# Kernel optimization log

Hardware: AMD Instinct MI355X
Metric: run time of the kernel (lower is better)

The kernel has to match this reference:

```python
import math
import jax, jax.numpy as jnp
import numpy as np

B, S, D, H = 4, 2048, 512, 8
DH = D // H
NUM_BUCKETS = 32
MAX_DISTANCE = 128


def _relative_position_bucket(rel_pos, num_buckets=NUM_BUCKETS, max_distance=MAX_DISTANCE):
    # bidirectional T5 bucketing (faithful to the torch staticmethod)
    num_buckets = num_buckets // 2
    rel_buckets = (rel_pos > 0).astype(jnp.int32) * num_buckets
    rel_pos = jnp.abs(rel_pos)
    max_exact = num_buckets // 2
    is_small = rel_pos < max_exact
    # clamp log arg to >=1 element to avoid -inf cast (masked out by is_small anyway)
    rp_f = jnp.maximum(rel_pos, 1).astype(jnp.float32)
    large = max_exact + (
        jnp.log(rp_f / max_exact) / math.log(max_distance / max_exact) * (num_buckets - max_exact)
    ).astype(jnp.int32)
    large = jnp.minimum(large, num_buckets - 1)
    return rel_buckets + jnp.where(is_small, rel_pos, large)


def setup_inputs() -> dict:
    rng = jax.random.key(0)
    ks = jax.random.split(rng, 12)
    s = 0.02
    return {
        'key':   jax.random.normal(ks[0], (B, S, D), jnp.float32),
        'value': jax.random.normal(ks[1], (B, S, D), jnp.float32),
        'query': jax.random.normal(ks[2], (B, S, D), jnp.float32),
        'Wq': jax.random.normal(ks[3], (D, D), jnp.float32) * s,
        'bq': jnp.zeros((D,), jnp.float32),
        'Wk': jax.random.normal(ks[4], (D, D), jnp.float32) * s,
        'bk': jnp.zeros((D,), jnp.float32),
        'Wv': jax.random.normal(ks[5], (D, D), jnp.float32) * s,
        'bv': jnp.zeros((D,), jnp.float32),
        'Wo': jax.random.normal(ks[6], (D, D), jnp.float32) * s,
        'bo': jnp.zeros((D,), jnp.float32),
        'rel_bias': jax.random.normal(ks[7], (NUM_BUCKETS, H), jnp.float32) * s,
        'mask': jax.random.bernoulli(ks[8], 0.5, (B, S, S)),
    }


def reference(key, value, query, Wq, bq, Wk, bk, Wv, bv, Wo, bo, rel_bias, mask):
    def shape(x):  # [B,S,D] -> [B,H,S,DH]
        return x.reshape(B, -1, H, DH).transpose(0, 2, 1, 3)

    q = shape(query @ Wq + bq) / math.sqrt(DH)
    k = shape(key @ Wk + bk)
    v = shape(value @ Wv + bv)

    scores = jnp.einsum('bhqd,bhkd->bhqk', q, k)  # [B,H,S,S]

    # T5 relative position bias
    rel_pos = jnp.arange(S)[None, :] - jnp.arange(S)[:, None]  # [S,S] memory - query
    buckets = _relative_position_bucket(rel_pos)
    pos_bias = rel_bias[buckets]                     # [S,S,H]
    scores = scores + pos_bias.transpose(2, 0, 1)[None]  # [1,H,S,S]

    scores = jnp.where(mask[:, None, :, :], jnp.float32(-1e18), scores)
    attn = jax.nn.softmax(scores, axis=-1)  # dropout p=0 -> identity

    ctx = jnp.einsum('bhqk,bhkd->bhqd', attn, v)
    ctx = ctx.transpose(0, 2, 1, 3).reshape(B, -1, D)
    return ctx @ Wo + bo
```

## Files before the change

### kernel.cpp

```cpp
#include <hip/hip_runtime.h>
#include <hip/hip_bf16.h>
#include <math.h>

#define BB 4
#define SS 2048
#define DD 512
#define HH 8
#define DHH 64
#define KPAD 72
#define GPAD 72
#define LOG2E 1.44269504088896340736f

typedef __attribute__((ext_vector_type(8))) short short8;
typedef __attribute__((ext_vector_type(4))) float f32x4;
typedef __attribute__((ext_vector_type(16))) float f32x16;
typedef __attribute__((ext_vector_type(4))) unsigned short ushort4v;
typedef unsigned short ushort;
typedef unsigned char uchar;
typedef unsigned int u32;
typedef unsigned long long u64;

static __device__ __forceinline__ ushort f2b(float x) {
    __hip_bfloat16 h = __float2bfloat16(x);
    return *reinterpret_cast<ushort*>(&h);
}

__global__ __launch_bounds__(256) void pack_mask_kernel(const void* __restrict__ mask,
                                                        u64* __restrict__ mwords) {
    __shared__ int sflag;
    const int tid = threadIdx.x;
    if (tid == 0) sflag = 0;
    __syncthreads();
    u32 probe = ((const u32*)mask)[tid];
    if (__any(probe > 1u) && (tid & 63) == 0) sflag = 1;
    __syncthreads();
    const bool bytemode = sflag != 0;

    int idx = blockIdx.x * 256 + tid;
    int w = idx & 31;
    int row = idx >> 5;
    u64 bits = 0ull;
    if (bytemode) {
        const uint4* p4 = (const uint4*)((const uchar*)mask + (size_t)row * SS + w * 64);
#pragma unroll
        for (int i = 0; i < 4; ++i) {
            uint4 v = p4[i];
            unsigned int a[4] = {v.x, v.y, v.z, v.w};
#pragma unroll
            for (int j = 0; j < 4; ++j)
#pragma unroll
                for (int byte = 0; byte < 4; ++byte)
                    if ((a[j] >> (byte * 8)) & 0xffu) bits |= 1ull << (i * 16 + j * 4 + byte);
        }
    } else {
        const int4* p4 = (const int4*)((const int*)mask + (size_t)row * SS + w * 64);
#pragma unroll
        for (int i = 0; i < 16; ++i) {
            int4 v = p4[i];
            if (v.x) bits |= 1ull << (i * 4 + 0);
            if (v.y) bits |= 1ull << (i * 4 + 1);
            if (v.z) bits |= 1ull << (i * 4 + 2);
            if (v.w) bits |= 1ull << (i * 4 + 3);
        }
    }
    mwords[idx] = bits;
}

__device__ __forceinline__ int t5_bucket(int rel) {
    int rb = (rel > 0) ? 16 : 0;
    int ap = rel < 0 ? -rel : rel;
    if (ap < 8) return rb + ap;
    float t = logf((float)ap * 0.125f) / 2.77258872985839844f * 8.0f;
    int large = 8 + (int)t;
    if (large > 15) large = 15;
    return rb + large;
}

__global__ __launch_bounds__(256) void bias_table_kernel(const float* __restrict__ rel_bias,
                                                         float* __restrict__ tbl) {
    int i = blockIdx.x * 256 + threadIdx.x;
    int h = i >> 12;
    int d = (i & 4095) - 2047;
    tbl[i] = LOG2E * rel_bias[t5_bucket(d) * HH + h];
}

__global__ __launch_bounds__(256) void wtrans_kernel(const float* __restrict__ W0, const float* __restrict__ W1,
                                                     const float* __restrict__ W2, const float* __restrict__ W3,
                                                     ushort* __restrict__ T0, ushort* __restrict__ T1,
                                                     ushort* __restrict__ T2, ushort* __restrict__ T3) {
    __shared__ float tile[64][65];
    const float* W = blockIdx.z == 0 ? W0 : blockIdx.z == 1 ? W1 : blockIdx.z == 2 ? W2 : W3;
    ushort*     T = blockIdx.z == 0 ? T0 : blockIdx.z == 1 ? T1 : blockIdx.z == 2 ? T2 : T3;
    const int n0 = blockIdx.x * 64, k0 = blockIdx.y * 64;
    const int tr = threadIdx.x >> 4, tc = threadIdx.x & 15;
#pragma unroll
    for (int i = 0; i < 4; ++i) {
        int r = i * 16 + tr;
        float4 v = *(const float4*)&W[(size_t)(k0 + r) * 512 + n0 + tc * 4];
        tile[r][tc * 4 + 0] = v.x; tile[r][tc * 4 + 1] = v.y;
        tile[r][tc * 4 + 2] = v.z; tile[r][tc * 4 + 3] = v.w;
    }
    __syncthreads();
#pragma unroll
    for (int i = 0; i < 4; ++i) {
        int rn = i * 16 + tr;
        ushort4v o;
#pragma unroll
        for (int j = 0; j < 4; ++j) o[j] = f2b(tile[tc * 4 + j][rn]);
        *(ushort4v*)&T[(size_t)(n0 + rn) * 512 + k0 + tc * 4] = o;
    }
}

__global__ __launch_bounds__(256) void qkv_gemm(const float* __restrict__ Xq, const float* __restrict__ Xk,
                                                const float* __restrict__ Xv,
                                                const ushort* __restrict__ Wqt, const ushort* __restrict__ Wkt,
                                                const ushort* __restrict__ Wvt,
                                                const float* __restrict__ bqp, const float* __restrict__ bkp,
                                                const float* __restrict__ bvp,
                                                ushort* __restrict__ Yq, ushort* __restrict__ Yk,
                                                ushort* __restrict__ Yv) {
    __shared__ ushort Als[128 * GPAD];
    __shared__ ushort Bls[128 * GPAD];
    const int z = blockIdx.z;
    const float* A    = z == 0 ? Xq : z == 1 ? Xk : Xv;
    const ushort* Bt  = z == 0 ? Wqt : z == 1 ? Wkt : Wvt;
    const float* bias = z == 0 ? bqp : z == 1 ? bkp : bvp;
    const float scale = z == 0 ? 0.125f * LOG2E : 1.0f;

    const int tid = threadIdx.x;
    const int lane = tid & 63;
    const int wid = tid >> 6;
    const int lq = lane & 15, lg = lane >> 4;
    const int wr = wid >> 1, wc = wid & 1;
    const int bm = blockIdx.x * 128;
    const int bn = blockIdx.y * 128;

    f32x4 acc[4][4];
#pragma unroll
    for (int m = 0; m < 4; ++m)
#pragma unroll
        for (int n = 0; n < 4; ++n) acc[m][n] = (f32x4){0.f, 0.f, 0.f, 0.f};

    const int sr = tid >> 3;
    const int sc = (tid & 7) * 8;

    for (int k0 = 0; k0 < 512; k0 += 64) {
        __syncthreads();
#pragma unroll
        for (int i = 0; i < 4; ++i) {
            int r = sr + i * 32;
            float4 u = *(const float4*)(A + (size_t)(bm + r) * 512 + k0 + sc);
            float4 v = *(const float4*)(A + (size_t)(bm + r) * 512 + k0 + sc + 4);
            short8 av;
            av[0] = (short)f2b(u.x); av[1] = (short)f2b(u.y); av[2] = (short)f2b(u.z); av[3] = (short)f2b(u.w);
            av[4] = (short)f2b(v.x); av[5] = (short)f2b(v.y); av[6] = (short)f2b(v.z); av[7] = (short)f2b(v.w);
            *(short8*)&Als[r * GPAD + sc] = av;
            short8 bv = *(const short8*)(Bt + (size_t)(bn + r) * 512 + k0 + sc);
            *(short8*)&Bls[r * GPAD + sc] = bv;
        }
        __syncthreads();
#pragma unroll
        for (int kk = 0; kk < 2; ++kk) {
            short8 af[4], bf[4];
#pragma unroll
            for (int m = 0; m < 4; ++m)
                af[m] = *(short8*)&Als[(wr * 64 + m * 16 + lq) * GPAD + kk * 32 + lg * 8];
#pragma unroll
            for (int n = 0; n < 4; ++n)
                bf[n] = *(short8*)&Bls[(wc * 64 + n * 16 + lq) * GPAD + kk * 32 + lg * 8];
#pragma unroll
            for (int m = 0; m < 4; ++m)
#pragma unroll
                for (int n = 0; n < 4; ++n)
                    acc[m][n] = __builtin_amdgcn_mfma_f32_16x16x32_bf16(af[m], bf[n], acc[m][n], 0, 0, 0);
        }
    }

    float bv[4];
#pragma unroll
    for (int n = 0; n < 4; ++n) bv[n] = bias[bn + wc * 64 + n * 16 + lq];

    if (z == 2) {
        const int blk = bm >> 11;
        const int s0 = (bm & 2047) + wr * 64 + lg * 4;
#pragma unroll
        for (int m = 0; m < 4; ++m)
#pragma unroll
            for (int n = 0; n < 4; ++n) {
                int col = bn + wc * 64 + n * 16 + lq;
                ushort4v o;
#pragma unroll
                for (int r = 0; r < 4; ++r) o[r] = f2b(acc[m][n][r] + bv[n]);
                *(ushort4v*)&Yv[((size_t)(blk * 512 + col)) * SS + s0 + m * 16] = o;
            }
    } else {
        ushort* Y = z ? Yk : Yq;
#pragma unroll
        for (int m = 0; m < 4; ++m)
#pragma unroll
            for (int r = 0; r < 4; ++r) {
                int row = bm + wr * 64 + m * 16 + lg * 4 + r;
#pragma unroll
                for (int n = 0; n < 4; ++n) {
                    int col = bn + wc * 64 + n * 16 + lq;
                    Y[(size_t)row * 512 + col] = f2b((acc[m][n][r] + bv[n]) * scale);
                }
            }
    }
}

__global__ __launch_bounds__(256) void out_gemm(const ushort* __restrict__ A,
                                                const ushort* __restrict__ Bt,
                                                const float* __restrict__ bias,
                                                float* __restrict__ Y) {
    __shared__ ushort Als[128 * GPAD];
    __shared__ ushort Bls[128 * GPAD];
    const int tid = threadIdx.x;
    const int lane = tid & 63;
    const int wid = tid >> 6;
    const int lq = lane & 15, lg = lane >> 4;
    const int wr = wid >> 1, wc = wid & 1;
    const int bm = blockIdx.x * 128;
    const int bn = blockIdx.y * 128;

    f32x4 acc[4][4];
#pragma unroll
    for (int m = 0; m < 4; ++m)
#pragma unroll
        for (int n = 0; n < 4; ++n) acc[m][n] = (f32x4){0.f, 0.f, 0.f, 0.f};

    const int sr = tid >> 3;
    const int sc = (tid & 7) * 8;

    for (int k0 = 0; k0 < 512; k0 += 64) {
        __syncthreads();
#pragma unroll
        for (int i = 0; i < 4; ++i) {
            int r = sr + i * 32;
            short8 av = *(const short8*)(A + (size_t)(bm + r) * 512 + k0 + sc);
            *(short8*)&Als[r * GPAD + sc] = av;
            short8 bv = *(const short8*)(Bt + (size_t)(bn + r) * 512 + k0 + sc);
            *(short8*)&Bls[r * GPAD + sc] = bv;
        }
        __syncthreads();
#pragma unroll
        for (int kk = 0; kk < 2; ++kk) {
            short8 af[4], bf[4];
#pragma unroll
            for (int m = 0; m < 4; ++m)
                af[m] = *(short8*)&Als[(wr * 64 + m * 16 + lq) * GPAD + kk * 32 + lg * 8];
#pragma unroll
            for (int n = 0; n < 4; ++n)
                bf[n] = *(short8*)&Bls[(wc * 64 + n * 16 + lq) * GPAD + kk * 32 + lg * 8];
#pragma unroll
            for (int m = 0; m < 4; ++m)
#pragma unroll
                for (int n = 0; n < 4; ++n)
                    acc[m][n] = __builtin_amdgcn_mfma_f32_16x16x32_bf16(af[m], bf[n], acc[m][n], 0, 0, 0);
        }
    }

    float bv[4];
#pragma unroll
    for (int n = 0; n < 4; ++n) bv[n] = bias[bn + wc * 64 + n * 16 + lq];
#pragma unroll
    for (int m = 0; m < 4; ++m)
#pragma unroll
        for (int r = 0; r < 4; ++r) {
            int row = bm + wr * 64 + m * 16 + lg * 4 + r;
#pragma unroll
            for (int n = 0; n < 4; ++n) {
                int col = bn + wc * 64 + n * 16 + lq;
                Y[(size_t)row * 512 + col] = acc[m][n][r] + bv[n];
            }
        }
}

__global__ __launch_bounds__(512, 4) void attn_kernel(const ushort* __restrict__ Qg, const ushort* __restrict__ Kg,
                                                      const ushort* __restrict__ vT, const u64* __restrict__ mwords,
                                                      const float* __restrict__ btbl, ushort* __restrict__ ctxb) {
    __shared__ ushort KV[4][64 * KPAD];
    __shared__ ushort QT[128 * KPAD];
    float* tbl = (float*)QT;

    const int bid = blockIdx.x;
    const int wk = ((bid & 7) << 6) | (bid >> 3);
    const int qb = wk & 15;
    const int h  = (wk >> 4) & 7;
    const int b  = wk >> 7;
    const int q0 = qb * 128;

    const int tid  = threadIdx.x;
    const int wid  = tid >> 6;
    const int lane = tid & 63;
    const int lq32 = lane & 31;
    const int hi   = lane >> 5;
    const int seg  = wid >> 2;
    const int qw   = wid & 3;

    const u64* mrow = mwords + (size_t)b * SS * 32;
    const int qg = q0 + qw * 32 + lq32;

    {
        const int r = tid >> 2;
        const int c = (tid & 3) * 16;
        const size_t g = ((size_t)(b * SS + q0 + r)) * DD + h * DHH + c;
        *(short8*)&QT[r * KPAD + c]     = *(const short8*)(Qg + g);
        *(short8*)&QT[r * KPAD + c + 8] = *(const short8*)(Qg + g + 8);
    }
    __syncthreads();

    short8 qf[4];
#pragma unroll
    for (int dch = 0; dch < 4; ++dch)
        qf[dch] = *(short8*)&QT[(qw * 32 + lq32) * KPAD + dch * 16 + hi * 8];
    __syncthreads();

    {
        const float4* src = (const float4*)(btbl + (size_t)h * 4096);
        float4* dst = (float4*)tbl;
        dst[tid]       = src[tid];
        dst[tid + 512] = src[tid + 512];
    }

    f32x16 acc0, acc1, accl;
#pragma unroll
    for (int i = 0; i < 16; ++i) { acc0[i] = 0.f; acc1[i] = 0.f; accl[i] = 0.f; }

    short8 ones;
#pragma unroll
    for (int i = 0; i < 8; ++i) ones[i] = (short)0x3F80;

    const int stile = tid >> 7;
    const int sidx = tid & 127;
    const int srow = sidx >> 1;
    const int scol = (sidx & 1) * 32;
    const size_t kbaseK = ((size_t)(b * SS + (stile & 1) * 1024 + srow)) * DD + h * DHH + scol;
    const size_t kbaseV = ((size_t)(b * DD + h * DHH + srow)) * SS + (stile & 1) * 1024 + scol;

    short8 stg[4];
    {
        const ushort* sp = (stile < 2) ? (Kg + kbaseK) : (vT + kbaseV);
#pragma unroll
        for (int j = 0; j < 4; ++j) stg[j] = *(const short8*)(sp + j * 8);
    }

    const float* tbp_base = tbl + (2047 + hi * 4 - qg);

    for (int t = 0; t < 16; ++t) {
        __syncthreads();
        {
            ushort* dst = &KV[stile][srow * KPAD + scol];
#pragma unroll
            for (int j = 0; j < 4; ++j) *(short8*)(dst + j * 8) = stg[j];
        }
        __syncthreads();
        if (t < 15) {
            const ushort* sp = (stile < 2) ? (Kg + kbaseK + (size_t)(t + 1) * 64 * DD)
                                           : (vT + kbaseV + (t + 1) * 64);
#pragma unroll
            for (int j = 0; j < 4; ++j) stg[j] = *(const short8*)(sp + j * 8);
        }

        const ushort* Ks = KV[seg];
        const ushort* Vt = KV[2 + seg];
        const int ktw = seg * 16 + t;
        const u64 wv = mrow[(size_t)qg * 32 + ktw];

        const float* tbp = tbp_base + ktw * 64;
        f32x16 st0, st1;
#pragma unroll
        for (int r = 0; r < 16; ++r) {
            const int br = (r & 3) + 8 * (r >> 2);
            st0[r] = tbp[br];
            st1[r] = tbp[32 + br];
        }
#pragma unroll
        for (int dch = 0; dch < 4; ++dch) {
            short8 kf0 = *(short8*)&Ks[lq32 * KPAD + dch * 16 + hi * 8];
            short8 kf1 = *(short8*)&Ks[(32 + lq32) * KPAD + dch * 16 + hi * 8];
            st0 = __builtin_amdgcn_mfma_f32_32x32x16_bf16(kf0, qf[dch], st0, 0, 0, 0);
            st1 = __builtin_amdgcn_mfma_f32_32x32x16_bf16(kf1, qf[dch], st1, 0, 0, 0);
        }

        const u32 mi0 = ~(((u32)wv) >> (hi * 4));
        const u32 mi1 = ~(((u32)(wv >> 32)) >> (hi * 4));
        float p0[16], p1[16];
#pragma unroll
        for (int r = 0; r < 16; ++r) {
            const int br = (r & 3) + 8 * (r >> 2);
            float e0 = __builtin_amdgcn_exp2f(st0[r]);
            float e1 = __builtin_amdgcn_exp2f(st1[r]);
            u32 k0 = (u32)(((int)(mi0 << (31 - br))) >> 31);
            u32 k1 = (u32)(((int)(mi1 << (31 - br))) >> 31);
            p0[r] = __uint_as_float(__float_as_uint(e0) & k0);
            p1[r] = __uint_as_float(__float_as_uint(e1) & k1);
        }

        u32 W[16];
#pragma unroll
        for (int w = 0; w < 8; ++w) {
            asm("v_cvt_pk_bf16_f32 %0, %1, %2" : "=v"(W[w])     : "v"(p0[2 * w]), "v"(p0[2 * w + 1]));
            asm("v_cvt_pk_bf16_f32 %0, %1, %2" : "=v"(W[8 + w]) : "v"(p1[2 * w]), "v"(p1[2 * w + 1]));
        }
        short8 pf[4];
#pragma unroll
        for (int g = 0; g < 4; ++g) {
            u32 A = W[g * 4 + 0], Bw = W[g * 4 + 1], C = W[g * 4 + 2], D = W[g * 4 + 3];
            asm("v_permlane32_swap_b32 %0, %1" : "+v"(A), "+v"(C));
            asm("v_permlane32_swap_b32 %0, %1" : "+v"(Bw), "+v"(D));
            u32 fr[4] = {A, Bw, C, D};
            pf[g] = *(short8*)fr;
        }

#pragma unroll
        for (int g = 0; g < 4; ++g) {
            short8 vf0 = *(short8*)&Vt[lq32 * KPAD + g * 16 + hi * 8];
            short8 vf1 = *(short8*)&Vt[(32 + lq32) * KPAD + g * 16 + hi * 8];
            acc0 = __builtin_amdgcn_mfma_f32_32x32x16_bf16(vf0, pf[g], acc0, 0, 0, 0);
            acc1 = __builtin_amdgcn_mfma_f32_32x32x16_bf16(vf1, pf[g], acc1, 0, 0, 0);
            accl = __builtin_amdgcn_mfma_f32_32x32x16_bf16(ones, pf[g], accl, 0, 0, 0);
        }
    }

    float l_run = accl[0];

    __syncthreads();
    float* cmb = (float*)KV;
    float* cl  = cmb + 128 * 65;
    const int q = qw * 32 + lq32;
    if (seg == 1) {
#pragma unroll
        for (int r = 0; r < 16; ++r) {
            const int dr = (r & 3) + 8 * (r >> 2) + 4 * hi;
            cmb[q * 65 + dr]      = acc0[r];
            cmb[q * 65 + 32 + dr] = acc1[r];
        }
        if (hi == 0) cl[q] = l_run;
    }
    __syncthreads();
    if (seg == 0) {
#pragma unroll
        for (int r = 0; r < 16; ++r) {
            const int dr = (r & 3) + 8 * (r >> 2) + 4 * hi;
            acc0[r] += cmb[q * 65 + dr];
            acc1[r] += cmb[q * 65 + 32 + dr];
        }
        l_run += cl[q];
        const float linv = 1.0f / l_run;
        ushort* T = QT;
#pragma unroll
        for (int r = 0; r < 16; ++r) {
            const int dr = (r & 3) + 8 * (r >> 2) + 4 * hi;
            T[q * KPAD + dr]      = f2b(acc0[r] * linv);
            T[q * KPAD + 32 + dr] = f2b(acc1[r] * linv);
        }
        const int r2 = qw * 32 + (lane >> 1);
        const int c0 = (lane & 1) * 32;
        const size_t g = ((size_t)(b * SS + q0 + r2)) * DD + h * DHH + c0;
#pragma unroll
        for (int j = 0; j < 4; ++j)
            *(short8*)(ctxb + g + j * 8) = *(short8*)&QT[r2 * KPAD + c0 + j * 8];
    }
}

extern "C" void kernel_launch(void* const* d_in, const int* in_sizes, int n_in,
                              void* d_out, int out_size, void* d_ws, size_t ws_size,
                              hipStream_t stream) {
    const float* key   = (const float*)d_in[0];
    const float* value = (const float*)d_in[1];
    const float* query = (const float*)d_in[2];
    const float* Wq = (const float*)d_in[3];
    const float* bq = (const float*)d_in[4];
    const float* Wk = (const float*)d_in[5];
    const float* bk = (const float*)d_in[6];
    const float* Wv = (const float*)d_in[7];
    const float* bv = (const float*)d_in[8];
    const float* Wo = (const float*)d_in[9];
    const float* bo = (const float*)d_in[10];
    const float* rel_bias = (const float*)d_in[11];
    const void* mask = d_in[12];
    float* out = (float*)d_out;

    char* ws = (char*)d_ws;
    const size_t MB = 1024 * 1024;
    float* btbl   = (float*)(ws + 4096);
    u64* mwords   = (u64*)(ws + 512 * 1024);
    ushort* wq_t  = (ushort*)(ws + (size_t)(3 * MB));
    ushort* wk_t  = wq_t + 512 * 512;
    ushort* wv_t  = wk_t + 512 * 512;
    ushort* wo_t  = wv_t + 512 * 512;
    ushort* q_bf  = (ushort*)(ws + (size_t)(5 * MB));
    ushort* k_bf  = q_bf + (size_t)8192 * 512;
    ushort* vT    = k_bf + (size_t)8192 * 512;
    ushort* ctx_bf = vT + (size_t)8192 * 512;

    hipLaunchKernelGGL(pack_mask_kernel, dim3(BB * SS * 32 / 256), dim3(256), 0, stream,
                       mask, mwords);
    hipLaunchKernelGGL(bias_table_kernel, dim3(HH * 4096 / 256), dim3(256), 0, stream,
                       rel_bias, btbl);
    hipLaunchKernelGGL(wtrans_kernel, dim3(8, 8, 4), dim3(256), 0, stream,
                       Wq, Wk, Wv, Wo, wq_t, wk_t, wv_t, wo_t);

    hipLaunchKernelGGL(qkv_gemm, dim3(64, 4, 3), dim3(256), 0, stream,
                       query, key, value, wq_t, wk_t, wv_t, bq, bk, bv, q_bf, k_bf, vT);

    hipLaunchKernelGGL(attn_kernel, dim3(512), dim3(512), 0, stream,
                       q_bf, k_bf, vT, mwords, btbl, ctx_bf);

    hipLaunchKernelGGL(out_gemm, dim3(64, 4), dim3(256), 0, stream, ctx_bf, wo_t, bo, out);
}
```

Before: 119.7 us.

## Load K/V MFMA fragments directly from global instead of staging through LDS

Drops the shared-memory double-staging of K and V tiles and the two per-iteration block barriers. Each wave now reads its K and V MFMA operand fragments straight from global memory (L2/L1), and Q is loaded directly into registers. This removes LDS write/read traffic and block-wide syncs from the main loop. In exchange, the four query waves in a segment each fetch the same K/V data redundantly, with smaller, less coalesced 16-byte loads and more exposed global latency.

```diff
diff --git a/kernel.cpp b/kernel.cpp
--- a/kernel.cpp
+++ b/kernel.cpp
@@ -279,9 +279,8 @@
 __global__ __launch_bounds__(512, 4) void attn_kernel(const ushort* __restrict__ Qg, const ushort* __restrict__ Kg,
                                                       const ushort* __restrict__ vT, const u64* __restrict__ mwords,
                                                       const float* __restrict__ btbl, ushort* __restrict__ ctxb) {
-    __shared__ ushort KV[4][64 * KPAD];
-    __shared__ ushort QT[128 * KPAD];
-    float* tbl = (float*)QT;
+    __shared__ float tbl[4096];
+    __shared__ float cmb[128 * 65 + 128];
 
     const int bid = blockIdx.x;
     const int wk = ((bid & 7) << 6) | (bid >> 3);
@@ -302,27 +301,18 @@
     const int qg = q0 + qw * 32 + lq32;
 
     {
-        const int r = tid >> 2;
-        const int c = (tid & 3) * 16;
-        const size_t g = ((size_t)(b * SS + q0 + r)) * DD + h * DHH + c;
-        *(short8*)&QT[r * KPAD + c]     = *(const short8*)(Qg + g);
-        *(short8*)&QT[r * KPAD + c + 8] = *(const short8*)(Qg + g + 8);
-    }
-    __syncthreads();
-
-    short8 qf[4];
-#pragma unroll
-    for (int dch = 0; dch < 4; ++dch)
-        qf[dch] = *(short8*)&QT[(qw * 32 + lq32) * KPAD + dch * 16 + hi * 8];
-    __syncthreads();
-
-    {
         const float4* src = (const float4*)(btbl + (size_t)h * 4096);
         float4* dst = (float4*)tbl;
         dst[tid]       = src[tid];
         dst[tid + 512] = src[tid + 512];
     }
 
+    const ushort* qrow = Qg + ((size_t)(b * SS + qg)) * DD + h * DHH;
+    short8 qf[4];
+#pragma unroll
+    for (int dch = 0; dch < 4; ++dch)
+        qf[dch] = *(const short8*)(qrow + dch * 16 + hi * 8);
+
     f32x16 acc0, acc1, accl;
 #pragma unroll
     for (int i = 0; i < 16; ++i) { acc0[i] = 0.f; acc1[i] = 0.f; accl[i] = 0.f; }
@@ -331,41 +321,28 @@
 #pragma unroll
     for (int i = 0; i < 8; ++i) ones[i] = (short)0x3F80;
 
-    const int stile = tid >> 7;
-    const int sidx = tid & 127;
-    const int srow = sidx >> 1;
-    const int scol = (sidx & 1) * 32;
-    const size_t kbaseK = ((size_t)(b * SS + (stile & 1) * 1024 + srow)) * DD + h * DHH + scol;
-    const size_t kbaseV = ((size_t)(b * DD + h * DHH + srow)) * SS + (stile & 1) * 1024 + scol;
-
-    short8 stg[4];
-    {
-        const ushort* sp = (stile < 2) ? (Kg + kbaseK) : (vT + kbaseV);
-#pragma unroll
-        for (int j = 0; j < 4; ++j) stg[j] = *(const short8*)(sp + j * 8);
-    }
+    const ushort* kbase = Kg + ((size_t)(b * SS + seg * 1024 + lq32)) * DD + h * DHH + hi * 8;
+    const ushort* vbase0 = vT + ((size_t)(b * DD + h * DHH + lq32)) * SS + seg * 1024 + hi * 8;
+    const ushort* vbase1 = vT + ((size_t)(b * DD + h * DHH + 32 + lq32)) * SS + seg * 1024 + hi * 8;
 
     const float* tbp_base = tbl + (2047 + hi * 4 - qg);
 
+    __syncthreads();
+
     for (int t = 0; t < 16; ++t) {
-        __syncthreads();
-        {
-            ushort* dst = &KV[stile][srow * KPAD + scol];
-#pragma unroll
-            for (int j = 0; j < 4; ++j) *(short8*)(dst + j * 8) = stg[j];
-        }
-        __syncthreads();
-        if (t < 15) {
-            const ushort* sp = (stile < 2) ? (Kg + kbaseK + (size_t)(t + 1) * 64 * DD)
-                                           : (vT + kbaseV + (t + 1) * 64);
-#pragma unroll
-            for (int j = 0; j < 4; ++j) stg[j] = *(const short8*)(sp + j * 8);
-        }
-
-        const ushort* Ks = KV[seg];
-        const ushort* Vt = KV[2 + seg];
         const int ktw = seg * 16 + t;
         const u64 wv = mrow[(size_t)qg * 32 + ktw];
+
+        short8 kf0[4], kf1[4];
+        {
+            const ushort* kp0 = kbase + (size_t)(t * 64) * DD;
+            const ushort* kp1 = kp0 + (size_t)32 * DD;
+#pragma unroll
+            for (int dch = 0; dch < 4; ++dch) {
+                kf0[dch] = *(const short8*)(kp0 + dch * 16);
+                kf1[dch] = *(const short8*)(kp1 + dch * 16);
+            }
+        }
 
         const float* tbp = tbp_base + ktw * 64;
         f32x16 st0, st1;
@@ -377,10 +354,15 @@
         }
 #pragma unroll
         for (int dch = 0; dch < 4; ++dch) {
-            short8 kf0 = *(short8*)&Ks[lq32 * KPAD + dch * 16 + hi * 8];
-            short8 kf1 = *(short8*)&Ks[(32 + lq32) * KPAD + dch * 16 + hi * 8];
-            st0 = __builtin_amdgcn_mfma_f32_32x32x16_bf16(kf0, qf[dch], st0, 0, 0, 0);
-            st1 = __builtin_amdgcn_mfma_f32_32x32x16_bf16(kf1, qf[dch], st1, 0, 0, 0);
+            st0 = __builtin_amdgcn_mfma_f32_32x32x16_bf16(kf0[dch], qf[dch], st0, 0, 0, 0);
+            st1 = __builtin_amdgcn_mfma_f32_32x32x16_bf16(kf1[dch], qf[dch], st1, 0, 0, 0);
+        }
+
+        short8 vf0[4], vf1[4];
+#pragma unroll
+        for (int g = 0; g < 4; ++g) {
+            vf0[g] = *(const short8*)(vbase0 + t * 64 + g * 16);
+            vf1[g] = *(const short8*)(vbase1 + t * 64 + g * 16);
         }
 
         const u32 mi0 = ~(((u32)wv) >> (hi * 4));
@@ -415,20 +397,16 @@
 
 #pragma unroll
         for (int g = 0; g < 4; ++g) {
-            short8 vf0 = *(short8*)&Vt[lq32 * KPAD + g * 16 + hi * 8];
-            short8 vf1 = *(short8*)&Vt[(32 + lq32) * KPAD + g * 16 + hi * 8];
-            acc0 = __builtin_amdgcn_mfma_f32_32x32x16_bf16(vf0, pf[g], acc0, 0, 0, 0);
-            acc1 = __builtin_amdgcn_mfma_f32_32x32x16_bf16(vf1, pf[g], acc1, 0, 0, 0);
+            acc0 = __builtin_amdgcn_mfma_f32_32x32x16_bf16(vf0[g], pf[g], acc0, 0, 0, 0);
+            acc1 = __builtin_amdgcn_mfma_f32_32x32x16_bf16(vf1[g], pf[g], acc1, 0, 0, 0);
             accl = __builtin_amdgcn_mfma_f32_32x32x16_bf16(ones, pf[g], accl, 0, 0, 0);
         }
     }
 
     float l_run = accl[0];
-
-    __syncthreads();
-    float* cmb = (float*)KV;
-    float* cl  = cmb + 128 * 65;
+    float* cl = cmb + 128 * 65;
     const int q = qw * 32 + lq32;
+
     if (seg == 1) {
 #pragma unroll
         for (int r = 0; r < 16; ++r) {
@@ -439,6 +417,7 @@
         if (hi == 0) cl[q] = l_run;
     }
     __syncthreads();
+    float linv = 0.f;
     if (seg == 0) {
 #pragma unroll
         for (int r = 0; r < 16; ++r) {
@@ -447,8 +426,11 @@
             acc1[r] += cmb[q * 65 + 32 + dr];
         }
         l_run += cl[q];
-        const float linv = 1.0f / l_run;
-        ushort* T = QT;
+        linv = 1.0f / l_run;
+    }
+    __syncthreads();
+    if (seg == 0) {
+        ushort* T = (ushort*)cmb;
 #pragma unroll
         for (int r = 0; r < 16; ++r) {
             const int dr = (r & 3) + 8 * (r >> 2) + 4 * hi;
@@ -460,7 +442,7 @@
         const size_t g = ((size_t)(b * SS + q0 + r2)) * DD + h * DHH + c0;
 #pragma unroll
         for (int j = 0; j < 4; ++j)
-            *(short8*)(ctxb + g + j * 8) = *(short8*)&QT[r2 * KPAD + c0 + j * 8];
+            *(short8*)(ctxb + g + j * 8) = *(short8*)&T[r2 * KPAD + c0 + j * 8];
     }
 }
 
```

Result: slower. 194.1 us (+62.2%).
